# Kernel tuning notes

Measured on AMD Instinct MI355X. Metric: run time of the kernel, lower is better.

## Reference

```python
import jax, jax.numpy as jnp
import numpy as np
import math

B, S, D, H = 4, 2048, 1024, 16
DK = D // H

def setup_inputs() -> dict:
    key = jax.random.key(0)
    ks = jax.random.split(key, 6)
    scale = 1.0 / math.sqrt(D)
    x = jax.random.normal(ks[0], (B, S, D), dtype=jnp.float32)
    mask = jnp.tril(jnp.ones((S, S), dtype=jnp.int32))[None, None]  # [1,1,S,S] causal
    Wq = jax.random.normal(ks[1], (D, D), dtype=jnp.float32) * scale
    Wk = jax.random.normal(ks[2], (D, D), dtype=jnp.float32) * scale
    Wv = jax.random.normal(ks[3], (D, D), dtype=jnp.float32) * scale
    Wo = jax.random.normal(ks[4], (D, D), dtype=jnp.float32) * scale
    z = jnp.zeros((D,), dtype=jnp.float32)
    return {"x": x, "mask": mask, "Wq": Wq, "bq": z, "Wk": Wk, "bk": z,
            "Wv": Wv, "bv": z, "Wo": Wo, "bo": z}

def reference(x, mask, Wq, bq, Wk, bk, Wv, bv, Wo, bo):
    bsz, seq_len, d_model = x.shape
    def split_heads(t):  # [B,S,D] -> [B,H,S,DK]
        return t.reshape(bsz, seq_len, H, DK).transpose(0, 2, 1, 3)
    Q = split_heads(x @ Wq + bq)
    K = split_heads(x @ Wk + bk)
    V = split_heads(x @ Wv + bv)
    scores = jnp.einsum('bhqd,bhkd->bhqk', Q, K) / jnp.sqrt(jnp.asarray(DK, x.dtype))
    scores = jnp.where(mask == 0, jnp.asarray(-jnp.inf, x.dtype), scores)
    attn = jax.nn.softmax(scores, axis=-1)
    # dropout is identity in eval mode
    context = jnp.einsum('bhqk,bhkd->bhqd', attn, V)
    context = context.transpose(0, 2, 1, 3).reshape(bsz, seq_len, d_model)
    return context @ Wo + bo
```

## Files before the change

### kernel.cpp

```cpp
#include <hip/hip_runtime.h>
#include <hip/hip_bf16.h>
#include <math.h>

#define BATCH 4
#define SEQ   2048
#define DMODEL 1024
#define NHEAD 16
#define DHEAD 64
#define MROWS (BATCH * SEQ)
#define SC_Q  0.1803368801111244f

typedef __attribute__((ext_vector_type(8))) short short8;
typedef __attribute__((ext_vector_type(4))) float f32x4;
typedef __attribute__((ext_vector_type(4))) unsigned short ushort4v;

__device__ inline unsigned short f2bf(float f) {
    union { float f; unsigned int u; } v; v.f = f;
    unsigned int r = v.u + 0x7FFFu + ((v.u >> 16) & 1u);
    return (unsigned short)(r >> 16);
}

__device__ inline unsigned int cvt_pk_bf16(float a, float b) {
    unsigned int r;
    asm("v_cvt_pk_bf16_f32 %0, %1, %2" : "=v"(r) : "v"(a), "v"(b));
    return r;
}

__device__ __forceinline__ void g2l16(const unsigned short* g, unsigned short* l) {
    __builtin_amdgcn_global_load_lds(
        (const __attribute__((address_space(1))) unsigned int*)g,
        (__attribute__((address_space(3))) unsigned int*)l, 16, 0, 0);
}

__global__ __launch_bounds__(256) void cvt_bf16_kernel(
    const float* __restrict__ src, unsigned short* __restrict__ dst, int n4)
{
    const int i = blockIdx.x * 256 + threadIdx.x;
    if (i < n4) {
        float4 v = ((const float4*)src)[i];
        ushort4v o = { f2bf(v.x), f2bf(v.y), f2bf(v.z), f2bf(v.w) };
        ((ushort4v*)dst)[i] = o;
    }
}

__global__ __launch_bounds__(256) void bias_pack_kernel(
    const float* __restrict__ bq, const float* __restrict__ bk,
    const float* __restrict__ bv, float* __restrict__ b3)
{
    const int i = blockIdx.x * 256 + threadIdx.x;
    if (i < DMODEL) {
        b3[i]              = bq[i];
        b3[i + DMODEL]     = bk[i];
        b3[i + 2 * DMODEL] = bv[i];
    }
}

__global__ __launch_bounds__(256) void transpose_cvt_kernel(
    const float* __restrict__ W0, const float* __restrict__ W1,
    const float* __restrict__ W2, const float* __restrict__ W3,
    unsigned short* __restrict__ T0, unsigned short* __restrict__ T1,
    unsigned short* __restrict__ T2, unsigned short* __restrict__ T3)
{
    const float* W; unsigned short* T;
    switch (blockIdx.z) {
        case 0: W = W0; T = T0; break;
        case 1: W = W1; T = T1; break;
        case 2: W = W2; T = T2; break;
        default: W = W3; T = T3; break;
    }
    __shared__ float tile[32][33];
    const int r0 = blockIdx.y * 32, c0 = blockIdx.x * 32;
    const int c = threadIdx.x & 31, r = threadIdx.x >> 5;
    #pragma unroll
    for (int i = 0; i < 4; ++i)
        tile[r + i * 8][c] = W[(size_t)(r0 + r + i * 8) * DMODEL + c0 + c];
    __syncthreads();
    #pragma unroll
    for (int i = 0; i < 4; ++i)
        T[(size_t)(c0 + r + i * 8) * DMODEL + r0 + c] = f2bf(tile[c][r + i * 8]);
}

__global__ __launch_bounds__(256) void transpose_v_kernel(
    const unsigned short* __restrict__ Vin, unsigned short* __restrict__ Vt)
{
    __shared__ unsigned short t[64][72];
    const int tid = threadIdx.x;
    const int kt = blockIdx.x, bh = blockIdx.y;
    const unsigned short* src = Vin + ((size_t)bh * SEQ + kt * 64) * DHEAD;
    const int r = tid >> 3, c = (tid & 7) * 8;
    *(short8*)&t[r][c]      = *(const short8*)(src + (size_t)r * DHEAD + c);
    *(short8*)&t[r + 32][c] = *(const short8*)(src + (size_t)(r + 32) * DHEAD + c);
    __syncthreads();
    unsigned short* dst = Vt + (size_t)bh * DHEAD * SEQ + kt * 64;
    const int d = tid >> 3, p0 = (tid & 7) * 8;
    short8 v0, v1;
    #pragma unroll
    for (int i = 0; i < 8; ++i) {
        const int p = p0 + i;
        const int k = (p & 32) | (((p >> 2) & 1) << 4) | (((p >> 3) & 3) << 2) | (p & 3);
        v0[i] = (short)t[k][d];
        v1[i] = (short)t[k][d + 32];
    }
    *(short8*)(dst + (size_t)d * SEQ + p0)        = v0;
    *(short8*)(dst + (size_t)(d + 32) * SEQ + p0) = v1;
}

__global__ __launch_bounds__(256) void gemm_qkv(
    const unsigned short* __restrict__ A, const unsigned short* __restrict__ Bt,
    const float* __restrict__ bias3, unsigned short* __restrict__ QKV )
{
    __shared__ unsigned short As[128 * 32];
    __shared__ unsigned short Bs[128 * 32];

    const int tid  = threadIdx.x;
    const int wave = tid >> 6, lane = tid & 63;
    const int l15  = lane & 15, quad = lane >> 4;
    const int wm   = (wave >> 1) * 64;
    const int wn   = (wave & 1) * 64;
    const int m0   = blockIdx.y * 128;
    const int n0   = blockIdx.x * 128;
    const int Kdim = DMODEL;

    f32x4 acc[4][4];
    #pragma unroll
    for (int i = 0; i < 4; ++i)
        #pragma unroll
        for (int j = 0; j < 4; ++j) acc[i][j] = (f32x4){0.f, 0.f, 0.f, 0.f};

    const int c_lo = wave * 64 + lane;

    for (int k0 = 0; k0 < Kdim; k0 += 32) {
        __syncthreads();
        {
            int c = c_lo;
            g2l16(A  + (size_t)(m0 + (c >> 2)) * Kdim + k0 + (c & 3) * 8, As + c * 8);
            g2l16(Bt + (size_t)(n0 + (c >> 2)) * Kdim + k0 + (c & 3) * 8, Bs + c * 8);
            c = c_lo + 256;
            g2l16(A  + (size_t)(m0 + (c >> 2)) * Kdim + k0 + (c & 3) * 8, As + c * 8);
            g2l16(Bt + (size_t)(n0 + (c >> 2)) * Kdim + k0 + (c & 3) * 8, Bs + c * 8);
        }
        __syncthreads();

        short8 af[4], bf[4];
        #pragma unroll
        for (int mi = 0; mi < 4; ++mi)
            af[mi] = *(const short8*)&As[(wm + mi * 16 + l15) * 32 + quad * 8];
        #pragma unroll
        for (int ni = 0; ni < 4; ++ni)
            bf[ni] = *(const short8*)&Bs[(wn + ni * 16 + l15) * 32 + quad * 8];
        #pragma unroll
        for (int mi = 0; mi < 4; ++mi)
            #pragma unroll
            for (int ni = 0; ni < 4; ++ni)
                acc[mi][ni] = __builtin_amdgcn_mfma_f32_16x16x32_bf16(
                    af[mi], bf[ni], acc[mi][ni], 0, 0, 0);
    }

    const size_t elems = (size_t)MROWS * DMODEL;
    #pragma unroll
    for (int mi = 0; mi < 4; ++mi) {
        #pragma unroll
        for (int r = 0; r < 4; ++r) {
            const int m = m0 + wm + mi * 16 + quad * 4 + r;
            const int b = m >> 11, s = m & 2047;
            #pragma unroll
            for (int ni = 0; ni < 4; ++ni) {
                const int n   = n0 + wn + ni * 16 + l15;
                const int seg = n >> 10, nn = n & 1023;
                const int h = nn >> 6, dk = nn & 63;
                const float sc  = (seg == 0) ? SC_Q : 1.0f;
                const float val = (acc[mi][ni][r] + bias3[n]) * sc;
                QKV[seg * elems + (((size_t)(b * NHEAD + h)) * SEQ + s) * DHEAD + dk] = f2bf(val);
            }
        }
    }
}

__global__ __launch_bounds__(256) void gemm_out(
    const unsigned short* __restrict__ A, const unsigned short* __restrict__ Bt,
    const float* __restrict__ bias, float* __restrict__ Cout)
{
    __shared__ unsigned short As[128 * 32];
    __shared__ unsigned short Bs[128 * 32];

    const int tid  = threadIdx.x;
    const int wave = tid >> 6, lane = tid & 63;
    const int l15  = lane & 15, quad = lane >> 4;
    const int wm   = (wave >> 1) * 64;
    const int wn   = (wave & 1) * 64;
    const int m0   = blockIdx.y * 128;
    const int n0   = blockIdx.x * 128;
    const int Kdim = DMODEL, Ndim = DMODEL;

    f32x4 acc[4][4];
    #pragma unroll
    for (int i = 0; i < 4; ++i)
        #pragma unroll
        for (int j = 0; j < 4; ++j) acc[i][j] = (f32x4){0.f, 0.f, 0.f, 0.f};

    const int c_lo = wave * 64 + lane;

    for (int k0 = 0; k0 < Kdim; k0 += 32) {
        __syncthreads();
        {
            int c = c_lo;
            g2l16(A  + (size_t)(m0 + (c >> 2)) * Kdim + k0 + (c & 3) * 8, As + c * 8);
            g2l16(Bt + (size_t)(n0 + (c >> 2)) * Kdim + k0 + (c & 3) * 8, Bs + c * 8);
            c = c_lo + 256;
            g2l16(A  + (size_t)(m0 + (c >> 2)) * Kdim + k0 + (c & 3) * 8, As + c * 8);
            g2l16(Bt + (size_t)(n0 + (c >> 2)) * Kdim + k0 + (c & 3) * 8, Bs + c * 8);
        }
        __syncthreads();

        short8 af[4], bf[4];
        #pragma unroll
        for (int mi = 0; mi < 4; ++mi)
            af[mi] = *(const short8*)&As[(wm + mi * 16 + l15) * 32 + quad * 8];
        #pragma unroll
        for (int ni = 0; ni < 4; ++ni)
            bf[ni] = *(const short8*)&Bs[(wn + ni * 16 + l15) * 32 + quad * 8];
        #pragma unroll
        for (int mi = 0; mi < 4; ++mi)
            #pragma unroll
            for (int ni = 0; ni < 4; ++ni)
                acc[mi][ni] = __builtin_amdgcn_mfma_f32_16x16x32_bf16(
                    af[mi], bf[ni], acc[mi][ni], 0, 0, 0);
    }

    #pragma unroll
    for (int mi = 0; mi < 4; ++mi) {
        #pragma unroll
        for (int r = 0; r < 4; ++r) {
            const int m = m0 + wm + mi * 16 + quad * 4 + r;
            #pragma unroll
            for (int ni = 0; ni < 4; ++ni) {
                const int n = n0 + wn + ni * 16 + l15;
                Cout[(size_t)m * Ndim + n] = acc[mi][ni][r] + bias[n];
            }
        }
    }
}

__global__ __launch_bounds__(256, 4) void attn_mfma7(
    const unsigned short* __restrict__ Q, const unsigned short* __restrict__ K,
    const unsigned short* __restrict__ VtG, unsigned short* __restrict__ ctx_out)
{
    __shared__ alignas(16) unsigned short Ks[2][64 * 64];
    __shared__ alignas(16) unsigned short Vs[2][64 * 64];

    const int tid  = threadIdx.x;
    const int wave = tid >> 6, lane = tid & 63;
    const int l15  = lane & 15, quad = lane >> 4;
    const int qa   = blockIdx.x;
    const int qb   = 31 - qa;
    const int bh   = blockIdx.y;
    const int b    = bh >> 4, h = bh & 15;

    const unsigned short* Kb0 = K   + (size_t)bh * SEQ * DHEAD;
    const unsigned short* Vb0 = VtG + (size_t)bh * DHEAD * SEQ;

    short8 qf[2][2];
    #pragma unroll
    for (int g = 0; g < 2; ++g) {
        const int qtile = g ? qb : qa;
        const unsigned short* qrow =
            Q + ((size_t)bh * SEQ + qtile * 64 + wave * 16 + l15) * DHEAD + quad * 8;
        qf[g][0] = *(const short8*)qrow;
        qf[g][1] = *(const short8*)(qrow + 32);
    }

    f32x4 Of[2][4];
    float lsum[2] = {0.f, 0.f};
    #pragma unroll
    for (int g = 0; g < 2; ++g)
        #pragma unroll
        for (int i = 0; i < 4; ++i) Of[g][i] = (f32x4){0.f, 0.f, 0.f, 0.f};

    const int qloc = wave * 16 + l15;
    const f32x4 zero4 = (f32x4){0.f, 0.f, 0.f, 0.f};

    const int ck0 = tid >> 3, cg0 = tid & 7;
    const int ck1 = (tid + 256) >> 3, cg1 = tid & 7;

    #define STAGE(buf, jb)                                                          \
        do {                                                                        \
            const unsigned short* Kt_ = Kb0 + (size_t)(jb) * 64 * DHEAD;            \
            const unsigned short* Vt_ = Vb0 + (jb) * 64;                            \
            g2l16(Kt_ + (size_t)ck0 * DHEAD + (cg0 ^ (ck0 & 7)) * 8,                \
                  &Ks[buf][(tid) * 8]);                                             \
            g2l16(Vt_ + (size_t)ck0 * SEQ   + (cg0 ^ (ck0 & 7)) * 8,                \
                  &Vs[buf][(tid) * 8]);                                             \
            g2l16(Kt_ + (size_t)ck1 * DHEAD + (cg1 ^ (ck1 & 7)) * 8,                \
                  &Ks[buf][(tid + 256) * 8]);                                       \
            g2l16(Vt_ + (size_t)ck1 * SEQ   + (cg1 ^ (ck1 & 7)) * 8,                \
                  &Vs[buf][(tid + 256) * 8]);                                       \
        } while (0)

    STAGE(0, 0);

    for (int jb = 0; jb <= qb; ++jb) {
        const int cur = jb & 1;
        asm volatile("s_waitcnt vmcnt(0)" ::: "memory");
        __syncthreads();
        if (jb < qb) STAGE(cur ^ 1, jb + 1);

        const bool act0  = (jb <= qa);
        const bool diag0 = (jb == qa);
        const bool diag1 = (jb == qb);
        const unsigned short* KsC = &Ks[cur][0];
        const unsigned short* VsC = &Vs[cur][0];

        union { unsigned int u[4]; short8 v; } pa[2][2];
        #pragma unroll
        for (int nt = 0; nt < 4; ++nt) {
            const int k = nt * 16 + l15;
            const short8 a0 = *(const short8*)&KsC[(k * 8 + ( quad      ^ (k & 7))) * 8];
            const short8 a1 = *(const short8*)&KsC[(k * 8 + ((quad + 4) ^ (k & 7))) * 8];

            f32x4 s1 = __builtin_amdgcn_mfma_f32_16x16x32_bf16(a0, qf[1][0], zero4, 0, 0, 0);
            s1       = __builtin_amdgcn_mfma_f32_16x16x32_bf16(a1, qf[1][1], s1,    0, 0, 0);
            f32x4 p1;
            #pragma unroll
            for (int r = 0; r < 4; ++r) p1[r] = __builtin_amdgcn_exp2f(s1[r]);
            if (diag1) {
                #pragma unroll
                for (int r = 0; r < 4; ++r)
                    if (nt * 16 + quad * 4 + r > qloc) p1[r] = 0.f;
            }
            lsum[1] += (p1[0] + p1[1]) + (p1[2] + p1[3]);
            pa[1][nt >> 1].u[(nt & 1) * 2]     = cvt_pk_bf16(p1[0], p1[1]);
            pa[1][nt >> 1].u[(nt & 1) * 2 + 1] = cvt_pk_bf16(p1[2], p1[3]);

            if (act0) {
                f32x4 s0 = __builtin_amdgcn_mfma_f32_16x16x32_bf16(a0, qf[0][0], zero4, 0, 0, 0);
                s0       = __builtin_amdgcn_mfma_f32_16x16x32_bf16(a1, qf[0][1], s0,    0, 0, 0);
                f32x4 p0;
                #pragma unroll
                for (int r = 0; r < 4; ++r) p0[r] = __builtin_amdgcn_exp2f(s0[r]);
                if (diag0) {
                    #pragma unroll
                    for (int r = 0; r < 4; ++r)
                        if (nt * 16 + quad * 4 + r > qloc) p0[r] = 0.f;
                }
                lsum[0] += (p0[0] + p0[1]) + (p0[2] + p0[3]);
                pa[0][nt >> 1].u[(nt & 1) * 2]     = cvt_pk_bf16(p0[0], p0[1]);
                pa[0][nt >> 1].u[(nt & 1) * 2 + 1] = cvt_pk_bf16(p0[2], p0[3]);
            }
        }

        #pragma unroll
        for (int cc = 0; cc < 2; ++cc) {
            #pragma unroll
            for (int nt = 0; nt < 4; ++nt) {
                const int d = nt * 16 + l15;
                const short8 vb = *(const short8*)
                    &VsC[(d * 8 + ((cc * 4 + quad) ^ (d & 7))) * 8];
                Of[1][nt] = __builtin_amdgcn_mfma_f32_16x16x32_bf16(
                    pa[1][cc].v, vb, Of[1][nt], 0, 0, 0);
                if (act0)
                    Of[0][nt] = __builtin_amdgcn_mfma_f32_16x16x32_bf16(
                        pa[0][cc].v, vb, Of[0][nt], 0, 0, 0);
            }
        }
    }
    #undef STAGE

    #pragma unroll
    for (int g = 0; g < 2; ++g) {
        const int qtile = g ? qb : qa;
        float l = lsum[g];
        l += __shfl_xor(l, 16);
        l += __shfl_xor(l, 32);
        #pragma unroll
        for (int r = 0; r < 4; ++r) {
            const float inv = 1.0f / __shfl(l, quad * 4 + r);
            const int s = qtile * 64 + wave * 16 + quad * 4 + r;
            unsigned short* o = ctx_out + ((size_t)(b * SEQ + s)) * DMODEL + h * DHEAD;
            #pragma unroll
            for (int nt = 0; nt < 4; ++nt)
                o[nt * 16 + l15] = f2bf(Of[g][nt][r] * inv);
        }
    }
}

extern "C" void kernel_launch(void* const* d_in, const int* in_sizes, int n_in,
                              void* d_out, int out_size, void* d_ws, size_t ws_size,
                              hipStream_t stream) {
    const float* x  = (const float*)d_in[0];
    const float* Wq = (const float*)d_in[2];
    const float* bq = (const float*)d_in[3];
    const float* Wk = (const float*)d_in[4];
    const float* bk = (const float*)d_in[5];
    const float* Wv = (const float*)d_in[6];
    const float* bv = (const float*)d_in[7];
    const float* Wo = (const float*)d_in[8];
    const float* bo = (const float*)d_in[9];
    float* out = (float*)d_out;

    const size_t elems  = (size_t)MROWS * DMODEL;
    const size_t welems = (size_t)DMODEL * DMODEL;
    unsigned short* xbf   = (unsigned short*)d_ws;
    unsigned short* WqkvT = xbf + elems;
    unsigned short* WoT   = WqkvT + 3 * welems;
    unsigned short* Qbuf  = WoT + welems;
    unsigned short* Kbuf  = Qbuf + elems;
    unsigned short* Vbuf  = Kbuf + elems;
    unsigned short* VtG   = Vbuf + elems;
    unsigned short* Cbuf  = VtG + elems;
    float*          bias3 = (float*)(Cbuf + elems);

    dim3 blk(256);

    cvt_bf16_kernel<<<dim3((int)(elems / 4 / 256)), blk, 0, stream>>>(x, xbf, (int)(elems / 4));
    transpose_cvt_kernel<<<dim3(32, 32, 4), blk, 0, stream>>>(
        Wq, Wk, Wv, Wo, WqkvT, WqkvT + welems, WqkvT + 2 * welems, WoT);
    bias_pack_kernel<<<dim3(4), blk, 0, stream>>>(bq, bk, bv, bias3);

    dim3 gqkv(3 * DMODEL / 128, MROWS / 128);
    gemm_qkv<<<gqkv, blk, 0, stream>>>(xbf, WqkvT, bias3, Qbuf);

    transpose_v_kernel<<<dim3(SEQ / 64, BATCH * NHEAD), blk, 0, stream>>>(Vbuf, VtG);

    dim3 gattn(16, BATCH * NHEAD);
    attn_mfma7<<<gattn, blk, 0, stream>>>(Qbuf, Kbuf, VtG, Cbuf);

    dim3 gout(DMODEL / 128, MROWS / 128);
    gemm_out<<<gout, blk, 0, stream>>>(Cbuf, WoT, bo, out);
}
```

Baseline: 289.7 us.

## Double-buffer LDS tiles and XCD-swizzle block order in projection GEMMs

Both the QKV and output projection GEMMs now use two LDS buffers. The next K-tile's global-to-LDS copy is issued before the MFMAs on the current tile, so the per-iteration syncs drop from two to one and load latency overlaps compute. Block indices are also remapped so that groups of consecutive workgroups (round-robined across the 8 XCDs) cover tiles in column-major order, aiming for better L2 reuse of the A/B tiles. The cost is doubled LDS per block, which may reduce occupancy, and the swizzle assumes the grid size is divisible by 8.

```diff
diff --git a/kernel.cpp b/kernel.cpp
--- a/kernel.cpp
+++ b/kernel.cpp
@@ -109,16 +109,21 @@
     const unsigned short* __restrict__ A, const unsigned short* __restrict__ Bt,
     const float* __restrict__ bias3, unsigned short* __restrict__ QKV )
 {
-    __shared__ unsigned short As[128 * 32];
-    __shared__ unsigned short Bs[128 * 32];
+    __shared__ unsigned short As[2][128 * 32];
+    __shared__ unsigned short Bs[2][128 * 32];
 
     const int tid  = threadIdx.x;
     const int wave = tid >> 6, lane = tid & 63;
     const int l15  = lane & 15, quad = lane >> 4;
     const int wm   = (wave >> 1) * 64;
     const int wn   = (wave & 1) * 64;
-    const int m0   = blockIdx.y * 128;
-    const int n0   = blockIdx.x * 128;
+
+    const int gx = gridDim.x, gy = gridDim.y;
+    const int orig = blockIdx.y * gx + blockIdx.x;
+    const int cpx  = (gx * gy) >> 3;
+    const int swz  = (orig & 7) * cpx + (orig >> 3);
+    const int m0   = (swz % gy) * 128;
+    const int n0   = (swz / gy) * 128;
     const int Kdim = DMODEL;
 
     f32x4 acc[4][4];
@@ -129,25 +134,33 @@
 
     const int c_lo = wave * 64 + lane;
 
-    for (int k0 = 0; k0 < Kdim; k0 += 32) {
+    #define GSTAGE(buf, k0)                                                               \
+        do {                                                                              \
+            int c = c_lo;                                                                 \
+            g2l16(A  + (size_t)(m0 + (c >> 2)) * Kdim + (k0) + (c & 3) * 8, &As[buf][c * 8]); \
+            g2l16(Bt + (size_t)(n0 + (c >> 2)) * Kdim + (k0) + (c & 3) * 8, &Bs[buf][c * 8]); \
+            c = c_lo + 256;                                                               \
+            g2l16(A  + (size_t)(m0 + (c >> 2)) * Kdim + (k0) + (c & 3) * 8, &As[buf][c * 8]); \
+            g2l16(Bt + (size_t)(n0 + (c >> 2)) * Kdim + (k0) + (c & 3) * 8, &Bs[buf][c * 8]); \
+        } while (0)
+
+    GSTAGE(0, 0);
+
+    for (int kt = 0; kt < Kdim / 32; ++kt) {
+        const int cur = kt & 1;
+        asm volatile("s_waitcnt vmcnt(0)" ::: "memory");
         __syncthreads();
-        {
-            int c = c_lo;
-            g2l16(A  + (size_t)(m0 + (c >> 2)) * Kdim + k0 + (c & 3) * 8, As + c * 8);
-            g2l16(Bt + (size_t)(n0 + (c >> 2)) * Kdim + k0 + (c & 3) * 8, Bs + c * 8);
-            c = c_lo + 256;
-            g2l16(A  + (size_t)(m0 + (c >> 2)) * Kdim + k0 + (c & 3) * 8, As + c * 8);
-            g2l16(Bt + (size_t)(n0 + (c >> 2)) * Kdim + k0 + (c & 3) * 8, Bs + c * 8);
-        }
-        __syncthreads();
-
+        if (kt < Kdim / 32 - 1) GSTAGE(cur ^ 1, (kt + 1) * 32);
+
+        const unsigned short* AsC = &As[cur][0];
+        const unsigned short* BsC = &Bs[cur][0];
         short8 af[4], bf[4];
         #pragma unroll
         for (int mi = 0; mi < 4; ++mi)
-            af[mi] = *(const short8*)&As[(wm + mi * 16 + l15) * 32 + quad * 8];
+            af[mi] = *(const short8*)&AsC[(wm + mi * 16 + l15) * 32 + quad * 8];
         #pragma unroll
         for (int ni = 0; ni < 4; ++ni)
-            bf[ni] = *(const short8*)&Bs[(wn + ni * 16 + l15) * 32 + quad * 8];
+            bf[ni] = *(const short8*)&BsC[(wn + ni * 16 + l15) * 32 + quad * 8];
         #pragma unroll
         for (int mi = 0; mi < 4; ++mi)
             #pragma unroll
@@ -155,6 +168,7 @@
                 acc[mi][ni] = __builtin_amdgcn_mfma_f32_16x16x32_bf16(
                     af[mi], bf[ni], acc[mi][ni], 0, 0, 0);
     }
+    #undef GSTAGE
 
     const size_t elems = (size_t)MROWS * DMODEL;
     #pragma unroll
@@ -180,16 +194,21 @@
     const unsigned short* __restrict__ A, const unsigned short* __restrict__ Bt,
     const float* __restrict__ bias, float* __restrict__ Cout)
 {
-    __shared__ unsigned short As[128 * 32];
-    __shared__ unsigned short Bs[128 * 32];
+    __shared__ unsigned short As[2][128 * 32];
+    __shared__ unsigned short Bs[2][128 * 32];
 
     const int tid  = threadIdx.x;
     const int wave = tid >> 6, lane = tid & 63;
     const int l15  = lane & 15, quad = lane >> 4;
     const int wm   = (wave >> 1) * 64;
     const int wn   = (wave & 1) * 64;
-    const int m0   = blockIdx.y * 128;
-    const int n0   = blockIdx.x * 128;
+
+    const int gx = gridDim.x, gy = gridDim.y;
+    const int orig = blockIdx.y * gx + blockIdx.x;
+    const int cpx  = (gx * gy) >> 3;
+    const int swz  = (orig & 7) * cpx + (orig >> 3);
+    const int m0   = (swz % gy) * 128;
+    const int n0   = (swz / gy) * 128;
     const int Kdim = DMODEL, Ndim = DMODEL;
 
     f32x4 acc[4][4];
@@ -200,25 +219,33 @@
 
     const int c_lo = wave * 64 + lane;
 
-    for (int k0 = 0; k0 < Kdim; k0 += 32) {
+    #define GSTAGE(buf, k0)                                                               \
+        do {                                                                              \
+            int c = c_lo;                                                                 \
+            g2l16(A  + (size_t)(m0 + (c >> 2)) * Kdim + (k0) + (c & 3) * 8, &As[buf][c * 8]); \
+            g2l16(Bt + (size_t)(n0 + (c >> 2)) * Kdim + (k0) + (c & 3) * 8, &Bs[buf][c * 8]); \
+            c = c_lo + 256;                                                               \
+            g2l16(A  + (size_t)(m0 + (c >> 2)) * Kdim + (k0) + (c & 3) * 8, &As[buf][c * 8]); \
+            g2l16(Bt + (size_t)(n0 + (c >> 2)) * Kdim + (k0) + (c & 3) * 8, &Bs[buf][c * 8]); \
+        } while (0)
+
+    GSTAGE(0, 0);
+
+    for (int kt = 0; kt < Kdim / 32; ++kt) {
+        const int cur = kt & 1;
+        asm volatile("s_waitcnt vmcnt(0)" ::: "memory");
         __syncthreads();
-        {
-            int c = c_lo;
-            g2l16(A  + (size_t)(m0 + (c >> 2)) * Kdim + k0 + (c & 3) * 8, As + c * 8);
-            g2l16(Bt + (size_t)(n0 + (c >> 2)) * Kdim + k0 + (c & 3) * 8, Bs + c * 8);
-            c = c_lo + 256;
-            g2l16(A  + (size_t)(m0 + (c >> 2)) * Kdim + k0 + (c & 3) * 8, As + c * 8);
-            g2l16(Bt + (size_t)(n0 + (c >> 2)) * Kdim + k0 + (c & 3) * 8, Bs + c * 8);
-        }
-        __syncthreads();
-
+        if (kt < Kdim / 32 - 1) GSTAGE(cur ^ 1, (kt + 1) * 32);
+
+        const unsigned short* AsC = &As[cur][0];
+        const unsigned short* BsC = &Bs[cur][0];
         short8 af[4], bf[4];
         #pragma unroll
         for (int mi = 0; mi < 4; ++mi)
-            af[mi] = *(const short8*)&As[(wm + mi * 16 + l15) * 32 + quad * 8];
+            af[mi] = *(const short8*)&AsC[(wm + mi * 16 + l15) * 32 + quad * 8];
         #pragma unroll
         for (int ni = 0; ni < 4; ++ni)
-            bf[ni] = *(const short8*)&Bs[(wn + ni * 16 + l15) * 32 + quad * 8];
+            bf[ni] = *(const short8*)&BsC[(wn + ni * 16 + l15) * 32 + quad * 8];
         #pragma unroll
         for (int mi = 0; mi < 4; ++mi)
             #pragma unroll
@@ -226,6 +253,7 @@
                 acc[mi][ni] = __builtin_amdgcn_mfma_f32_16x16x32_bf16(
                     af[mi], bf[ni], acc[mi][ni], 0, 0, 0);
     }
+    #undef GSTAGE
 
     #pragma unroll
     for (int mi = 0; mi < 4; ++mi) {
```

Result: slower. 299.6 us (+3.4%).

## Double-buffer LDS in QKV and output GEMMs to overlap loads with MFMA

Applied to the files above, without the earlier changes.

Both projection GEMMs now use two LDS buffers per operand. The global-to-LDS copy for the next K-slice is issued before the MFMAs on the current slice, so memory latency overlaps compute, and each K-step needs only one barrier instead of two. Precomputed global pointers are advanced incrementally, and launch bounds add a minimum of 4 blocks per CU. The cost is doubled LDS (32KB per block) and a waitcnt vmcnt(0) at each step, which still serializes on the in-flight loads.

```diff
diff --git a/kernel.cpp b/kernel.cpp
--- a/kernel.cpp
+++ b/kernel.cpp
@@ -105,56 +105,77 @@
     *(short8*)(dst + (size_t)(d + 32) * SEQ + p0) = v1;
 }
 
-__global__ __launch_bounds__(256) void gemm_qkv(
+#define GEMM_PRE()                                                             \
+    __shared__ unsigned short As[2][128 * 32];                                 \
+    __shared__ unsigned short Bs[2][128 * 32];                                 \
+    const int tid  = threadIdx.x;                                              \
+    const int wave = tid >> 6, lane = tid & 63;                                \
+    const int l15  = lane & 15, quad = lane >> 4;                              \
+    const int wm   = (wave >> 1) * 64;                                         \
+    const int wn   = (wave & 1) * 64;                                          \
+    const int m0   = blockIdx.y * 128;                                         \
+    const int n0   = blockIdx.x * 128;                                         \
+    f32x4 acc[4][4];                                                           \
+    _Pragma("unroll")                                                          \
+    for (int i = 0; i < 4; ++i)                                                \
+        _Pragma("unroll")                                                      \
+        for (int j = 0; j < 4; ++j) acc[i][j] = (f32x4){0.f, 0.f, 0.f, 0.f};   \
+    const int c1 = tid + 256;                                                  \
+    const unsigned short* gA0 = A  + (size_t)(m0 + (tid >> 2)) * DMODEL + (tid & 3) * 8; \
+    const unsigned short* gB0 = Bt + (size_t)(n0 + (tid >> 2)) * DMODEL + (tid & 3) * 8; \
+    const unsigned short* gA1 = A  + (size_t)(m0 + (c1 >> 2))  * DMODEL + (c1 & 3) * 8;  \
+    const unsigned short* gB1 = Bt + (size_t)(n0 + (c1 >> 2))  * DMODEL + (c1 & 3) * 8;  \
+    unsigned short* const dA00 = &As[0][tid * 8];                              \
+    unsigned short* const dB00 = &Bs[0][tid * 8];                              \
+    unsigned short* const dA10 = &As[0][c1 * 8];                               \
+    unsigned short* const dB10 = &Bs[0][c1 * 8];                               \
+    unsigned short* const dA01 = &As[1][tid * 8];                              \
+    unsigned short* const dB01 = &Bs[1][tid * 8];                              \
+    unsigned short* const dA11 = &As[1][c1 * 8];                               \
+    unsigned short* const dB11 = &Bs[1][c1 * 8];
+
+#define GSTAGE(dA0, dB0, dA1, dB1)                                             \
+    do { g2l16(gA0, dA0); g2l16(gB0, dB0); g2l16(gA1, dA1); g2l16(gB1, dB1);   \
+         gA0 += 32; gB0 += 32; gA1 += 32; gB1 += 32; } while (0)
+
+#define GCOMP(buf)                                                             \
+    do {                                                                       \
+        short8 af[4], bfr[4];                                                  \
+        _Pragma("unroll")                                                      \
+        for (int mi = 0; mi < 4; ++mi)                                         \
+            af[mi] = *(const short8*)&As[buf][(wm + mi * 16 + l15) * 32 + quad * 8]; \
+        _Pragma("unroll")                                                      \
+        for (int ni = 0; ni < 4; ++ni)                                         \
+            bfr[ni] = *(const short8*)&Bs[buf][(wn + ni * 16 + l15) * 32 + quad * 8]; \
+        _Pragma("unroll")                                                      \
+        for (int mi = 0; mi < 4; ++mi)                                         \
+            _Pragma("unroll")                                                  \
+            for (int ni = 0; ni < 4; ++ni)                                     \
+                acc[mi][ni] = __builtin_amdgcn_mfma_f32_16x16x32_bf16(         \
+                    af[mi], bfr[ni], acc[mi][ni], 0, 0, 0);                    \
+    } while (0)
+
+#define GLOOP()                                                                \
+    GSTAGE(dA00, dB00, dA10, dB10);                        \
+    _Pragma("unroll 1")                                                        \
+    for (int kt = 0; kt < DMODEL / 32; kt += 2) {                              \
+        asm volatile("s_waitcnt vmcnt(0)" ::: "memory");                       \
+        __syncthreads();                                                       \
+        GSTAGE(dA01, dB01, dA11, dB11);                 \
+        GCOMP(0);                                                              \
+        asm volatile("s_waitcnt vmcnt(0)" ::: "memory");                       \
+        __syncthreads();                                                       \
+        if (kt + 2 < DMODEL / 32)                                              \
+            GSTAGE(dA00, dB00, dA10, dB10);             \
+        GCOMP(1);                                                              \
+    }
+
+__global__ __launch_bounds__(256, 4) void gemm_qkv(
     const unsigned short* __restrict__ A, const unsigned short* __restrict__ Bt,
     const float* __restrict__ bias3, unsigned short* __restrict__ QKV )
 {
-    __shared__ unsigned short As[128 * 32];
-    __shared__ unsigned short Bs[128 * 32];
-
-    const int tid  = threadIdx.x;
-    const int wave = tid >> 6, lane = tid & 63;
-    const int l15  = lane & 15, quad = lane >> 4;
-    const int wm   = (wave >> 1) * 64;
-    const int wn   = (wave & 1) * 64;
-    const int m0   = blockIdx.y * 128;
-    const int n0   = blockIdx.x * 128;
-    const int Kdim = DMODEL;
-
-    f32x4 acc[4][4];
-    #pragma unroll
-    for (int i = 0; i < 4; ++i)
-        #pragma unroll
-        for (int j = 0; j < 4; ++j) acc[i][j] = (f32x4){0.f, 0.f, 0.f, 0.f};
-
-    const int c_lo = wave * 64 + lane;
-
-    for (int k0 = 0; k0 < Kdim; k0 += 32) {
-        __syncthreads();
-        {
-            int c = c_lo;
-            g2l16(A  + (size_t)(m0 + (c >> 2)) * Kdim + k0 + (c & 3) * 8, As + c * 8);
-            g2l16(Bt + (size_t)(n0 + (c >> 2)) * Kdim + k0 + (c & 3) * 8, Bs + c * 8);
-            c = c_lo + 256;
-            g2l16(A  + (size_t)(m0 + (c >> 2)) * Kdim + k0 + (c & 3) * 8, As + c * 8);
-            g2l16(Bt + (size_t)(n0 + (c >> 2)) * Kdim + k0 + (c & 3) * 8, Bs + c * 8);
-        }
-        __syncthreads();
-
-        short8 af[4], bf[4];
-        #pragma unroll
-        for (int mi = 0; mi < 4; ++mi)
-            af[mi] = *(const short8*)&As[(wm + mi * 16 + l15) * 32 + quad * 8];
-        #pragma unroll
-        for (int ni = 0; ni < 4; ++ni)
-            bf[ni] = *(const short8*)&Bs[(wn + ni * 16 + l15) * 32 + quad * 8];
-        #pragma unroll
-        for (int mi = 0; mi < 4; ++mi)
-            #pragma unroll
-            for (int ni = 0; ni < 4; ++ni)
-                acc[mi][ni] = __builtin_amdgcn_mfma_f32_16x16x32_bf16(
-                    af[mi], bf[ni], acc[mi][ni], 0, 0, 0);
-    }
+    GEMM_PRE();
+    GLOOP();
 
     const size_t elems = (size_t)MROWS * DMODEL;
     #pragma unroll
@@ -176,56 +197,12 @@
     }
 }
 
-__global__ __launch_bounds__(256) void gemm_out(
+__global__ __launch_bounds__(256, 4) void gemm_out(
     const unsigned short* __restrict__ A, const unsigned short* __restrict__ Bt,
     const float* __restrict__ bias, float* __restrict__ Cout)
 {
-    __shared__ unsigned short As[128 * 32];
-    __shared__ unsigned short Bs[128 * 32];
-
-    const int tid  = threadIdx.x;
-    const int wave = tid >> 6, lane = tid & 63;
-    const int l15  = lane & 15, quad = lane >> 4;
-    const int wm   = (wave >> 1) * 64;
-    const int wn   = (wave & 1) * 64;
-    const int m0   = blockIdx.y * 128;
-    const int n0   = blockIdx.x * 128;
-    const int Kdim = DMODEL, Ndim = DMODEL;
-
-    f32x4 acc[4][4];
-    #pragma unroll
-    for (int i = 0; i < 4; ++i)
-        #pragma unroll
-        for (int j = 0; j < 4; ++j) acc[i][j] = (f32x4){0.f, 0.f, 0.f, 0.f};
-
-    const int c_lo = wave * 64 + lane;
-
-    for (int k0 = 0; k0 < Kdim; k0 += 32) {
-        __syncthreads();
-        {
-            int c = c_lo;
-            g2l16(A  + (size_t)(m0 + (c >> 2)) * Kdim + k0 + (c & 3) * 8, As + c * 8);
-            g2l16(Bt + (size_t)(n0 + (c >> 2)) * Kdim + k0 + (c & 3) * 8, Bs + c * 8);
-            c = c_lo + 256;
-            g2l16(A  + (size_t)(m0 + (c >> 2)) * Kdim + k0 + (c & 3) * 8, As + c * 8);
-            g2l16(Bt + (size_t)(n0 + (c >> 2)) * Kdim + k0 + (c & 3) * 8, Bs + c * 8);
-        }
-        __syncthreads();
-
-        short8 af[4], bf[4];
-        #pragma unroll
-        for (int mi = 0; mi < 4; ++mi)
-            af[mi] = *(const short8*)&As[(wm + mi * 16 + l15) * 32 + quad * 8];
-        #pragma unroll
-        for (int ni = 0; ni < 4; ++ni)
-            bf[ni] = *(const short8*)&Bs[(wn + ni * 16 + l15) * 32 + quad * 8];
-        #pragma unroll
-        for (int mi = 0; mi < 4; ++mi)
-            #pragma unroll
-            for (int ni = 0; ni < 4; ++ni)
-                acc[mi][ni] = __builtin_amdgcn_mfma_f32_16x16x32_bf16(
-                    af[mi], bf[ni], acc[mi][ni], 0, 0, 0);
-    }
+    GEMM_PRE();
+    GLOOP();
 
     #pragma unroll
     for (int mi = 0; mi < 4; ++mi) {
@@ -235,7 +212,7 @@
             #pragma unroll
             for (int ni = 0; ni < 4; ++ni) {
                 const int n = n0 + wn + ni * 16 + l15;
-                Cout[(size_t)m * Ndim + n] = acc[mi][ni][r] + bias[n];
+                Cout[(size_t)m * DMODEL + n] = acc[mi][ni][r] + bias[n];
             }
         }
     }
```

After: 285.7 us. About the same (-1.4%).

## Double-buffer GEMMs with 256x128 tiles, K-step 64 and swizzled LDS

Applied to the files above, without the earlier changes.

Replaces both projection GEMM main loops with a shared 512-thread routine that uses 256x128 block tiles and a K-step of 64. Global-to-LDS loads are double-buffered with explicit vmcnt waits, so the next stage's loads overlap the current stage's MFMAs. An XOR swizzle on LDS columns avoids bank conflicts. The larger LDS footprint (96KB) limits blocks per CU, and the output GEMM grid shrinks to 256 blocks.

```diff
diff --git a/kernel.cpp b/kernel.cpp
--- a/kernel.cpp
+++ b/kernel.cpp
@@ -105,56 +105,108 @@
     *(short8*)(dst + (size_t)(d + 32) * SEQ + p0) = v1;
 }
 
-__global__ __launch_bounds__(256) void gemm_qkv(
+__device__ __forceinline__ void gemm_main_256x128(
+    const unsigned short* __restrict__ A, const unsigned short* __restrict__ Bt,
+    f32x4 (&acc)[4][4], int m0, int n0, int wm, int wn, int l15, int quad)
+{
+    __shared__ unsigned short As[2][256 * 64];
+    __shared__ unsigned short Bs[2][128 * 64];
+
+    const int tid = threadIdx.x;
+
+    #pragma unroll
+    for (int i = 0; i < 4; ++i)
+        #pragma unroll
+        for (int j = 0; j < 4; ++j) acc[i][j] = (f32x4){0.f, 0.f, 0.f, 0.f};
+
+    const unsigned short* gA[4];
+    const unsigned short* gB[2];
+    #pragma unroll
+    for (int j = 0; j < 4; ++j) {
+        const int c = tid + j * 512, row = c >> 3, gq = (c & 7) ^ (row & 7);
+        gA[j] = A + (size_t)(m0 + row) * DMODEL + gq * 8;
+    }
+    #pragma unroll
+    for (int j = 0; j < 2; ++j) {
+        const int c = tid + j * 512, row = c >> 3, gq = (c & 7) ^ (row & 7);
+        gB[j] = Bt + (size_t)(n0 + row) * DMODEL + gq * 8;
+    }
+
+    #define STAGE2(buf)                                                        \
+        do {                                                                   \
+            _Pragma("unroll")                                                  \
+            for (int j = 0; j < 4; ++j) {                                      \
+                g2l16(gA[j], &As[buf][(tid + j * 512) * 8]); gA[j] += 64;      \
+            }                                                                  \
+            _Pragma("unroll")                                                  \
+            for (int j = 0; j < 2; ++j) {                                      \
+                g2l16(gB[j], &Bs[buf][(tid + j * 512) * 8]); gB[j] += 64;      \
+            }                                                                  \
+        } while (0)
+
+    STAGE2(0);
+
+    const int NT = DMODEL / 64;
+    #pragma unroll 2
+    for (int t = 0; t < NT; ++t) {
+        const int cur = t & 1;
+        if (t + 1 < NT) {
+            STAGE2(cur ^ 1);
+            asm volatile("s_waitcnt vmcnt(6)" ::: "memory");
+        } else {
+            asm volatile("s_waitcnt vmcnt(0)" ::: "memory");
+        }
+        __syncthreads();
+
+        short8 bfr[4][2];
+        #pragma unroll
+        for (int ni = 0; ni < 4; ++ni) {
+            const int row = wn + ni * 16 + l15;
+            const unsigned short* bp = &Bs[cur][row * 64];
+            bfr[ni][0] = *(const short8*)(bp + ((    quad) ^ (row & 7)) * 8);
+            bfr[ni][1] = *(const short8*)(bp + ((4 + quad) ^ (row & 7)) * 8);
+        }
+        #pragma unroll
+        for (int pp = 0; pp < 2; ++pp) {
+            short8 af[2][2];
+            #pragma unroll
+            for (int mm = 0; mm < 2; ++mm) {
+                const int row = wm + (pp * 2 + mm) * 16 + l15;
+                const unsigned short* ap = &As[cur][row * 64];
+                af[mm][0] = *(const short8*)(ap + ((    quad) ^ (row & 7)) * 8);
+                af[mm][1] = *(const short8*)(ap + ((4 + quad) ^ (row & 7)) * 8);
+            }
+            __builtin_amdgcn_s_setprio(1);
+            #pragma unroll
+            for (int mm = 0; mm < 2; ++mm)
+                #pragma unroll
+                for (int ni = 0; ni < 4; ++ni) {
+                    acc[pp * 2 + mm][ni] = __builtin_amdgcn_mfma_f32_16x16x32_bf16(
+                        af[mm][0], bfr[ni][0], acc[pp * 2 + mm][ni], 0, 0, 0);
+                    acc[pp * 2 + mm][ni] = __builtin_amdgcn_mfma_f32_16x16x32_bf16(
+                        af[mm][1], bfr[ni][1], acc[pp * 2 + mm][ni], 0, 0, 0);
+                }
+            __builtin_amdgcn_s_setprio(0);
+        }
+        __syncthreads();
+    }
+    #undef STAGE2
+}
+
+__global__ __launch_bounds__(512, 2) void gemm_qkv(
     const unsigned short* __restrict__ A, const unsigned short* __restrict__ Bt,
     const float* __restrict__ bias3, unsigned short* __restrict__ QKV )
 {
-    __shared__ unsigned short As[128 * 32];
-    __shared__ unsigned short Bs[128 * 32];
-
     const int tid  = threadIdx.x;
     const int wave = tid >> 6, lane = tid & 63;
     const int l15  = lane & 15, quad = lane >> 4;
     const int wm   = (wave >> 1) * 64;
     const int wn   = (wave & 1) * 64;
-    const int m0   = blockIdx.y * 128;
+    const int m0   = blockIdx.y * 256;
     const int n0   = blockIdx.x * 128;
-    const int Kdim = DMODEL;
 
     f32x4 acc[4][4];
-    #pragma unroll
-    for (int i = 0; i < 4; ++i)
-        #pragma unroll
-        for (int j = 0; j < 4; ++j) acc[i][j] = (f32x4){0.f, 0.f, 0.f, 0.f};
-
-    const int c_lo = wave * 64 + lane;
-
-    for (int k0 = 0; k0 < Kdim; k0 += 32) {
-        __syncthreads();
-        {
-            int c = c_lo;
-            g2l16(A  + (size_t)(m0 + (c >> 2)) * Kdim + k0 + (c & 3) * 8, As + c * 8);
-            g2l16(Bt + (size_t)(n0 + (c >> 2)) * Kdim + k0 + (c & 3) * 8, Bs + c * 8);
-            c = c_lo + 256;
-            g2l16(A  + (size_t)(m0 + (c >> 2)) * Kdim + k0 + (c & 3) * 8, As + c * 8);
-            g2l16(Bt + (size_t)(n0 + (c >> 2)) * Kdim + k0 + (c & 3) * 8, Bs + c * 8);
-        }
-        __syncthreads();
-
-        short8 af[4], bf[4];
-        #pragma unroll
-        for (int mi = 0; mi < 4; ++mi)
-            af[mi] = *(const short8*)&As[(wm + mi * 16 + l15) * 32 + quad * 8];
-        #pragma unroll
-        for (int ni = 0; ni < 4; ++ni)
-            bf[ni] = *(const short8*)&Bs[(wn + ni * 16 + l15) * 32 + quad * 8];
-        #pragma unroll
-        for (int mi = 0; mi < 4; ++mi)
-            #pragma unroll
-            for (int ni = 0; ni < 4; ++ni)
-                acc[mi][ni] = __builtin_amdgcn_mfma_f32_16x16x32_bf16(
-                    af[mi], bf[ni], acc[mi][ni], 0, 0, 0);
-    }
+    gemm_main_256x128(A, Bt, acc, m0, n0, wm, wn, l15, quad);
 
     const size_t elems = (size_t)MROWS * DMODEL;
     #pragma unroll
@@ -176,56 +228,20 @@
     }
 }
 
-__global__ __launch_bounds__(256) void gemm_out(
+__global__ __launch_bounds__(512, 2) void gemm_out(
     const unsigned short* __restrict__ A, const unsigned short* __restrict__ Bt,
     const float* __restrict__ bias, float* __restrict__ Cout)
 {
-    __shared__ unsigned short As[128 * 32];
-    __shared__ unsigned short Bs[128 * 32];
-
     const int tid  = threadIdx.x;
     const int wave = tid >> 6, lane = tid & 63;
     const int l15  = lane & 15, quad = lane >> 4;
     const int wm   = (wave >> 1) * 64;
     const int wn   = (wave & 1) * 64;
-    const int m0   = blockIdx.y * 128;
+    const int m0   = blockIdx.y * 256;
     const int n0   = blockIdx.x * 128;
-    const int Kdim = DMODEL, Ndim = DMODEL;
 
     f32x4 acc[4][4];
-    #pragma unroll
-    for (int i = 0; i < 4; ++i)
-        #pragma unroll
-        for (int j = 0; j < 4; ++j) acc[i][j] = (f32x4){0.f, 0.f, 0.f, 0.f};
-
-    const int c_lo = wave * 64 + lane;
-
-    for (int k0 = 0; k0 < Kdim; k0 += 32) {
-        __syncthreads();
-        {
-            int c = c_lo;
-            g2l16(A  + (size_t)(m0 + (c >> 2)) * Kdim + k0 + (c & 3) * 8, As + c * 8);
-            g2l16(Bt + (size_t)(n0 + (c >> 2)) * Kdim + k0 + (c & 3) * 8, Bs + c * 8);
-            c = c_lo + 256;
-            g2l16(A  + (size_t)(m0 + (c >> 2)) * Kdim + k0 + (c & 3) * 8, As + c * 8);
-            g2l16(Bt + (size_t)(n0 + (c >> 2)) * Kdim + k0 + (c & 3) * 8, Bs + c * 8);
-        }
-        __syncthreads();
-
-        short8 af[4], bf[4];
-        #pragma unroll
-        for (int mi = 0; mi < 4; ++mi)
-            af[mi] = *(const short8*)&As[(wm + mi * 16 + l15) * 32 + quad * 8];
-        #pragma unroll
-        for (int ni = 0; ni < 4; ++ni)
-            bf[ni] = *(const short8*)&Bs[(wn + ni * 16 + l15) * 32 + quad * 8];
-        #pragma unroll
-        for (int mi = 0; mi < 4; ++mi)
-            #pragma unroll
-            for (int ni = 0; ni < 4; ++ni)
-                acc[mi][ni] = __builtin_amdgcn_mfma_f32_16x16x32_bf16(
-                    af[mi], bf[ni], acc[mi][ni], 0, 0, 0);
-    }
+    gemm_main_256x128(A, Bt, acc, m0, n0, wm, wn, l15, quad);
 
     #pragma unroll
     for (int mi = 0; mi < 4; ++mi) {
@@ -235,7 +251,7 @@
             #pragma unroll
             for (int ni = 0; ni < 4; ++ni) {
                 const int n = n0 + wn + ni * 16 + l15;
-                Cout[(size_t)m * Ndim + n] = acc[mi][ni][r] + bias[n];
+                Cout[(size_t)m * DMODEL + n] = acc[mi][ni][r] + bias[n];
             }
         }
     }
@@ -410,20 +426,21 @@
     float*          bias3 = (float*)(Cbuf + elems);
 
     dim3 blk(256);
+    dim3 blk2(512);
 
     cvt_bf16_kernel<<<dim3((int)(elems / 4 / 256)), blk, 0, stream>>>(x, xbf, (int)(elems / 4));
     transpose_cvt_kernel<<<dim3(32, 32, 4), blk, 0, stream>>>(
         Wq, Wk, Wv, Wo, WqkvT, WqkvT + welems, WqkvT + 2 * welems, WoT);
     bias_pack_kernel<<<dim3(4), blk, 0, stream>>>(bq, bk, bv, bias3);
 
-    dim3 gqkv(3 * DMODEL / 128, MROWS / 128);
-    gemm_qkv<<<gqkv, blk, 0, stream>>>(xbf, WqkvT, bias3, Qbuf);
+    dim3 gqkv(3 * DMODEL / 128, MROWS / 256);
+    gemm_qkv<<<gqkv, blk2, 0, stream>>>(xbf, WqkvT, bias3, Qbuf);
 
     transpose_v_kernel<<<dim3(SEQ / 64, BATCH * NHEAD), blk, 0, stream>>>(Vbuf, VtG);
 
     dim3 gattn(16, BATCH * NHEAD);
     attn_mfma7<<<gattn, blk, 0, stream>>>(Qbuf, Kbuf, VtG, Cbuf);
 
-    dim3 gout(DMODEL / 128, MROWS / 128);
-    gemm_out<<<gout, blk, 0, stream>>>(Cbuf, WoT, bo, out);
-}
+    dim3 gout(DMODEL / 128, MROWS / 256);
+    gemm_out<<<gout, blk2, 0, stream>>>(Cbuf, WoT, bo, out);
+}
```

Result: slower. 295.7 us (+2.1%).
